# Kernel tuning notes

Measured on AMD Instinct MI355X. Metric: run time of the kernel, lower is better.

## Reference

```python
import jax, jax.numpy as jnp
import numpy as np

N_NODES = 50000
IN_CH = 512
HID = 256
HEADS = 4
N_LAYERS = 2
LN_EPS = 1e-5


def _layer_norm(x, g, b):
    mu = jnp.mean(x, axis=-1, keepdims=True)
    var = jnp.mean((x - mu) ** 2, axis=-1, keepdims=True)
    return (x - mu) * jax.lax.rsqrt(var + LN_EPS) * g + b


def _trans_conv(x, wq, bq, wk, bk, wv, bv):
    # x: [N, HID]; projections -> [N, HEADS, HID]
    N = x.shape[0]
    qs = (x @ wq + bq).reshape(N, HEADS, HID)
    ks = (x @ wk + bk).reshape(N, HEADS, HID)
    vs = (x @ wv + bv).reshape(N, HEADS, HID)
    # NOTE: global Frobenius norm, matching torch.norm(t, p=2)
    qs = qs / jnp.linalg.norm(qs)
    ks = ks / jnp.linalg.norm(ks)
    kvs = jnp.einsum('lhm,lhd->hmd', ks, vs)                 # [H, C, C]
    attn_num = jnp.einsum('nhm,hmd->nhd', qs, kvs) + N * vs  # [N, H, C]
    ks_sum = jnp.sum(ks, axis=0)                             # [H, C]
    denom = jnp.einsum('nhm,hm->nh', qs, ks_sum)[..., None] + N
    return jnp.mean(attn_num / denom, axis=1)                # [N, HID]


def setup_inputs() -> dict:
    key = jax.random.key(0)
    ks = jax.random.split(key, 32)
    s_in = 1.0 / np.sqrt(IN_CH)
    s_h = 1.0 / np.sqrt(HID)
    inp = {
        'x': jax.random.normal(ks[0], (N_NODES, IN_CH), jnp.float32),
        'fc_w': jax.random.uniform(ks[1], (IN_CH, HID), jnp.float32, -s_in, s_in),
        'fc_b': jax.random.uniform(ks[2], (HID,), jnp.float32, -s_in, s_in),
        'ln0_g': jnp.ones((HID,), jnp.float32),
        'ln0_b': jnp.zeros((HID,), jnp.float32),
    }
    for i in range(N_LAYERS):
        base = 3 + i * 8
        inp[f'wq{i}'] = jax.random.uniform(ks[base + 0], (HID, HID * HEADS), jnp.float32, -s_h, s_h)
        inp[f'bq{i}'] = jax.random.uniform(ks[base + 1], (HID * HEADS,), jnp.float32, -s_h, s_h)
        inp[f'wk{i}'] = jax.random.uniform(ks[base + 2], (HID, HID * HEADS), jnp.float32, -s_h, s_h)
        inp[f'bk{i}'] = jax.random.uniform(ks[base + 3], (HID * HEADS,), jnp.float32, -s_h, s_h)
        inp[f'wv{i}'] = jax.random.uniform(ks[base + 4], (HID, HID * HEADS), jnp.float32, -s_h, s_h)
        inp[f'bv{i}'] = jax.random.uniform(ks[base + 5], (HID * HEADS,), jnp.float32, -s_h, s_h)
        inp[f'ln{i + 1}_g'] = jnp.ones((HID,), jnp.float32)
        inp[f'ln{i + 1}_b'] = jnp.zeros((HID,), jnp.float32)
    return inp


def reference(x, fc_w, fc_b, ln0_g, ln0_b,
              wq0, bq0, wk0, bk0, wv0, bv0, ln1_g, ln1_b,
              wq1, bq1, wk1, bk1, wv1, bv1, ln2_g, ln2_b):
    # input FFN path (ffn is hard-coded True); dropout is identity in eval mode
    h = jax.nn.relu(_layer_norm(x @ fc_w + fc_b, ln0_g, ln0_b))
    layers = [(wq0, bq0, wk0, bk0, wv0, bv0, ln1_g, ln1_b),
              (wq1, bq1, wk1, bk1, wv1, bv1, ln2_g, ln2_b)]
    for (wq, bq, wk, bk, wv, bv, g, b) in layers:
        prev = h
        h = _trans_conv(h, wq, bq, wk, bk, wv, bv)
        h = (h + prev) / 2.0
        h = jax.nn.relu(_layer_norm(h, g, b))
    return h
```

## Files before the change

### kernel.cpp

```cpp
#include <hip/hip_runtime.h>

#define NN    50000
#define IN_CH 512
#define HID   256
#define PJ    1024
#define FN    50000.0f
#define KTP   50176
#define NCH   98
#define CHK   512

typedef __attribute__((ext_vector_type(4)))  float f32x4;
typedef __attribute__((ext_vector_type(16))) float f32x16;
typedef __attribute__((ext_vector_type(4)))  int   i32x4;
typedef __attribute__((ext_vector_type(8)))  unsigned short u16x8;

__device__ inline void mfma16(f32x4& c, i32x4 a, i32x4 b){
  asm("v_mfma_f32_16x16x32_bf16 %0, %1, %2, %0" : "+v"(c) : "v"(a), "v"(b));
}
__device__ inline void mfma32(f32x16& c, i32x4 a, i32x4 b){
  asm("v_mfma_f32_32x32x16_bf16 %0, %1, %2, %0" : "+v"(c) : "v"(a), "v"(b));
}

__device__ inline unsigned short f2bf(float f){
  unsigned int u = __builtin_bit_cast(unsigned int, f);
  unsigned int r = (u + 0x7fffu + ((u >> 16) & 1u)) >> 16;
  return (unsigned short)r;
}
__device__ inline float bf2f(unsigned short u){
  unsigned int x = ((unsigned int)u) << 16;
  return __builtin_bit_cast(float, x);
}

__device__ inline float wave_reduce(float v){
  #pragma unroll
  for(int o=32;o>0;o>>=1) v += __shfl_down(v,o,64);
  return v;
}
__device__ inline float block_reduce(float v, float* sh4){
  v = wave_reduce(v);
  int lane = threadIdx.x & 63, wv = threadIdx.x >> 6;
  if(lane==0) sh4[wv] = v;
  __syncthreads();
  float r = sh4[0]+sh4[1]+sh4[2]+sh4[3];
  __syncthreads();
  return r;
}

__global__ void wconv(const float* __restrict__ w, unsigned short* __restrict__ wt){
  int idx = blockIdx.x*256 + threadIdx.x;
  if(idx >= IN_CH*HID) return;
  int k = idx >> 8, n = idx & 255;
  wt[((size_t)(k>>6)*256 + n)*64 + (k&63)] = f2bf(w[idx]);
}

__global__ __launch_bounds__(512)
void ffn_gemm(const float* __restrict__ X, const unsigned short* __restrict__ FWT2,
              const float* __restrict__ bias, const float* __restrict__ g,
              const float* __restrict__ b2, unsigned short* __restrict__ hbo){
  __shared__ __align__(16) unsigned char smem[55296];
  unsigned short (*as)[72] = (unsigned short(*)[72])smem;
  unsigned short (*bs)[72] = (unsigned short(*)[72])(smem + 18432);
  int t = threadIdx.x;
  int bm = blockIdx.x*128;
  int w = t>>6, lane = t&63;
  int wr = w>>2, wc = w&3;
  f32x4 acc[4][4];
  #pragma unroll
  for(int i=0;i<4;i++)
    #pragma unroll
    for(int j=0;j<4;j++) acc[i][j] = (f32x4){0.f,0.f,0.f,0.f};

  int ar = t>>2, aq = t&3;
  bool aok = (bm+ar) < NN;
  const float* xsrc = X + (size_t)(bm+ar)*IN_CH + aq*16;
  ushort4 aregs[4];
  u16x8 bregs[4];
  #pragma unroll
  for(int i=0;i<4;i++){
    float4 v = aok ? *(const float4*)(xsrc + i*4) : make_float4(0.f,0.f,0.f,0.f);
    ushort4 u; u.x=f2bf(v.x); u.y=f2bf(v.y); u.z=f2bf(v.z); u.w=f2bf(v.w);
    aregs[i]=u;
  }
  #pragma unroll
  for(int i=0;i<4;i++) bregs[i] = *(const u16x8*)(FWT2 + (size_t)t*32 + i*8);

  for(int kb=0;kb<8;kb++){
    __syncthreads();
    #pragma unroll
    for(int i=0;i<4;i++) *(ushort4*)&as[ar][aq*16 + i*4] = aregs[i];
    { int n = t>>1, q = t&1;
      #pragma unroll
      for(int i=0;i<4;i++) *(u16x8*)&bs[n][q*32 + i*8] = bregs[i];
    }
    __syncthreads();
    if(kb<7){
      const float* xs2 = xsrc + (kb+1)*64;
      #pragma unroll
      for(int i=0;i<4;i++){
        float4 v = aok ? *(const float4*)(xs2 + i*4) : make_float4(0.f,0.f,0.f,0.f);
        ushort4 u; u.x=f2bf(v.x); u.y=f2bf(v.y); u.z=f2bf(v.z); u.w=f2bf(v.w);
        aregs[i]=u;
      }
      const unsigned short* bsrc = FWT2 + (size_t)(kb+1)*16384 + (size_t)t*32;
      #pragma unroll
      for(int i=0;i<4;i++) bregs[i] = *(const u16x8*)(bsrc + i*8);
    }
    #pragma unroll
    for(int ks=0;ks<2;ks++){
      i32x4 af[4], bfv[4];
      #pragma unroll
      for(int i=0;i<4;i++) af[i]  = *(const i32x4*)&as[wr*64 + i*16 + (lane&15)][ks*32 + (lane>>4)*8];
      #pragma unroll
      for(int j=0;j<4;j++) bfv[j] = *(const i32x4*)&bs[wc*64 + j*16 + (lane&15)][ks*32 + (lane>>4)*8];
      #pragma unroll
      for(int i=0;i<4;i++)
        #pragma unroll
        for(int j=0;j<4;j++) mfma16(acc[i][j], af[i], bfv[j]);
    }
  }
  __syncthreads();
  int cb = wc*64;
  #pragma unroll
  for(int j=0;j<4;j++){
    float bb = bias[cb + j*16 + (lane&15)];
    #pragma unroll
    for(int i=0;i<4;i++)
      #pragma unroll
      for(int r=0;r<4;r++) acc[i][j][r] += bb;
  }
  float (*lnp)[4][2] = (float(*)[4][2])smem;
  float (*lnstat)[2] = (float(*)[2])(smem + 4096);
  #pragma unroll
  for(int i=0;i<4;i++)
    #pragma unroll
    for(int r=0;r<4;r++){
      float s=0.f, q=0.f;
      #pragma unroll
      for(int j=0;j<4;j++){ float a=acc[i][j][r]; s+=a; q+=a*a; }
      #pragma unroll
      for(int m=1;m<16;m<<=1){ s += __shfl_xor(s,m,64); q += __shfl_xor(q,m,64); }
      if((lane&15)==0){
        int row = wr*64 + i*16 + (lane>>4)*4 + r;
        lnp[row][wc][0]=s; lnp[row][wc][1]=q;
      }
    }
  __syncthreads();
  if(t<128){
    float s=0.f,q=0.f;
    #pragma unroll
    for(int c=0;c<4;c++){ s+=lnp[t][c][0]; q+=lnp[t][c][1]; }
    float mu = s*(1.f/HID);
    float var = q*(1.f/HID) - mu*mu;
    lnstat[t][0]=mu; lnstat[t][1]=rsqrtf(var+1e-5f);
  }
  __syncthreads();
  #pragma unroll
  for(int j=0;j<4;j++){
    int col = cb + j*16 + (lane&15);
    float gg = g[col], bb = b2[col];
    #pragma unroll
    for(int i=0;i<4;i++)
      #pragma unroll
      for(int r=0;r<4;r++){
        int row = wr*64 + i*16 + (lane>>4)*4 + r;
        int grow = bm + row;
        if(grow<NN){
          float y = fmaxf((acc[i][j][r]-lnstat[row][0])*lnstat[row][1]*gg + bb, 0.f);
          hbo[(size_t)grow*HID + col] = f2bf(y);
        }
      }
  }
}

__global__ void ln_relu2b(const unsigned short* __restrict__ in, const float* __restrict__ g,
                          const float* __restrict__ b, unsigned short* __restrict__ outb,
                          float* __restrict__ outf, int M){
  int lane = threadIdx.x & 63, wv = threadIdx.x >> 6;
  int row = blockIdx.x*4 + wv;
  if(row>=M) return;
  const unsigned short* rp = in + (size_t)row*HID;
  ushort4 hv = *(const ushort4*)(rp + lane*4);
  float v[4] = {bf2f(hv.x), bf2f(hv.y), bf2f(hv.z), bf2f(hv.w)};
  float sum = v[0]+v[1]+v[2]+v[3];
  float sq  = v[0]*v[0]+v[1]*v[1]+v[2]*v[2]+v[3]*v[3];
  sum = wave_reduce(sum); sq = wave_reduce(sq);
  sum = __shfl(sum,0,64); sq = __shfl(sq,0,64);
  float mu = sum*(1.f/HID);
  float var = sq*(1.f/HID) - mu*mu;
  float rs = rsqrtf(var + 1e-5f);
  float y[4];
  #pragma unroll
  for(int j=0;j<4;j++){ int c=lane*4+j;
    y[j] = fmaxf((v[j]-mu)*rs*g[c] + b[c], 0.f); }
  if(outb){
    ushort4 u; u.x=f2bf(y[0]); u.y=f2bf(y[1]); u.z=f2bf(y[2]); u.w=f2bf(y[3]);
    *(ushort4*)(outb + (size_t)row*HID + lane*4) = u;
  }
  if(outf){
    float4 f; f.x=y[0]; f.y=y[1]; f.z=y[2]; f.w=y[3];
    *(float4*)(outf + (size_t)row*HID + lane*4) = f;
  }
}

__global__ __launch_bounds__(256)
void transpose_h(const unsigned short* __restrict__ hb, unsigned short* __restrict__ ht){
  __shared__ unsigned short ts[64][72];
  int r0 = blockIdx.x*64, c0 = blockIdx.y*64;
  int t = threadIdx.x;
  { int r = t&63, q = t>>6;
    #pragma unroll
    for(int i=0;i<2;i++){
      int c = q*16 + i*8;
      u16x8 v = {0,0,0,0,0,0,0,0};
      if(r0+r < NN) v = *(const u16x8*)(hb + (size_t)(r0+r)*HID + c0 + c);
      *(u16x8*)&ts[r][c] = v;
    }
  }
  __syncthreads();
  { int c = t>>2, q = t&3;
    unsigned short tmp[16];
    #pragma unroll
    for(int i=0;i<16;i++) tmp[i] = ts[q*16+i][c];
    unsigned short* dst = ht + (size_t)(c0+c)*KTP + r0 + q*16;
    *(u16x8*)(dst)   = *(u16x8*)&tmp[0];
    *(u16x8*)(dst+8) = *(u16x8*)&tmp[8];
  }
}

__global__ __launch_bounds__(256)
void gram_mfma(const unsigned short* __restrict__ ht, float* __restrict__ gp){
  const int qmap[3] = {0,1,3};
  int qi = blockIdx.x, q = qmap[qi], ch = blockIdx.y;
  __shared__ unsigned short as[128][72], bs[128][72];
  int r0 = (q>>1)*128, c0 = (q&1)*128;
  int t = threadIdx.x, w=t>>6, lane=t&63;
  int wr=w>>1, wc=w&1;
  f32x4 acc[4][4];
  #pragma unroll
  for(int i=0;i<4;i++)
    #pragma unroll
    for(int j=0;j<4;j++) acc[i][j] = (f32x4){0.f,0.f,0.f,0.f};
  size_t kbase = (size_t)ch*CHK;
  for(int k0=0;k0<CHK;k0+=64){
    { int r = t>>1, h2 = t&1;
      const unsigned short* srcA = ht + (size_t)(r0+r)*KTP + kbase + k0 + h2*32;
      const unsigned short* srcB = ht + (size_t)(c0+r)*KTP + kbase + k0 + h2*32;
      #pragma unroll
      for(int i=0;i<4;i++) *(u16x8*)&as[r][h2*32+i*8] = *(const u16x8*)(srcA + i*8);
      #pragma unroll
      for(int i=0;i<4;i++) *(u16x8*)&bs[r][h2*32+i*8] = *(const u16x8*)(srcB + i*8);
    }
    __syncthreads();
    #pragma unroll
    for(int ks=0;ks<2;ks++){
      i32x4 af[4], bfv[4];
      #pragma unroll
      for(int i=0;i<4;i++) af[i]  = *(const i32x4*)&as[wr*64 + i*16 + (lane&15)][ks*32 + (lane>>4)*8];
      #pragma unroll
      for(int j=0;j<4;j++) bfv[j] = *(const i32x4*)&bs[wc*64 + j*16 + (lane&15)][ks*32 + (lane>>4)*8];
      #pragma unroll
      for(int i=0;i<4;i++)
        #pragma unroll
        for(int j=0;j<4;j++) mfma16(acc[i][j], af[i], bfv[j]);
    }
    __syncthreads();
  }
  float* dst = gp + ((size_t)qi*NCH + ch)*16384;
  #pragma unroll
  for(int i=0;i<4;i++)
    #pragma unroll
    for(int j=0;j<4;j++)
      #pragma unroll
      for(int r=0;r<4;r++)
        dst[(wr*64+i*16+(lane>>4)*4+r)*128 + wc*64+j*16+(lane&15)] = acc[i][j][r];
}

__global__ void gram_post(const float* __restrict__ gp, float* __restrict__ G,
                          const unsigned short* __restrict__ ht, float* __restrict__ svec){
  int b = blockIdx.x;
  if(b < 192){
    int qi = b>>6; int e = (b&63)*256 + threadIdx.x;
    const float* p = gp + (size_t)qi*NCH*16384 + e;
    float s=0.f;
    for(int c=0;c<NCH;c++) s += p[(size_t)c*16384];
    int i = e>>7, j = e&127;
    int r0 = (qi==2)?128:0, c0 = (qi==0)?0:128;
    G[(r0+i)*256 + c0+j] = s;
    if(qi==1) G[(c0+j)*256 + (r0+i)] = s;
  } else {
    int row = b - 192;
    const unsigned short* p = ht + (size_t)row*KTP;
    float s = 0.f;
    for(int i = threadIdx.x*8; i < KTP; i += 2048){
      u16x8 v = *(const u16x8*)(p + i);
      #pragma unroll
      for(int e=0;e<8;e++) s += bf2f(v[e]);
    }
    __shared__ float sh4[4];
    float tot = block_reduce(s, sh4);
    if(threadIdx.x==0) svec[row] = tot;
  }
}

__global__ void gw_gemm3(const float* __restrict__ G, const float* __restrict__ Wq,
                         const float* __restrict__ Wk, const float* __restrict__ Wv,
                         float* __restrict__ gw){
  const float* B = blockIdx.z==0?Wq:(blockIdx.z==1?Wk:Wv);
  float* C = gw + (size_t)blockIdx.z*262144;
  __shared__ float As[64][33];
  __shared__ float Bs[32][64];
  int bm = blockIdx.x*64, bn = blockIdx.y*64;
  int t = threadIdx.x;
  int tn = t & 15, tm = t >> 4;
  float acc[4][4] = {};
  for(int k0=0;k0<HID;k0+=32){
    { int kk=t&31, rr=t>>5;
      #pragma unroll
      for(int p=0;p<8;p++){ int r=rr+p*8;
        As[r][kk] = G[(size_t)(bm+r)*HID + k0+kk]; } }
    { int nn=t&63, kr=t>>6;
      #pragma unroll
      for(int p=0;p<8;p++){ int k=kr+p*4;
        Bs[k][nn] = B[(size_t)(k0+k)*PJ + bn+nn]; } }
    __syncthreads();
    for(int k=0;k<32;k++){
      float a[4], b[4];
      #pragma unroll
      for(int i=0;i<4;i++) a[i]=As[tm*4+i][k];
      #pragma unroll
      for(int j=0;j<4;j++) b[j]=Bs[k][tn*4+j];
      #pragma unroll
      for(int i=0;i<4;i++)
        #pragma unroll
        for(int j=0;j<4;j++) acc[i][j] += a[i]*b[j];
    }
    __syncthreads();
  }
  #pragma unroll
  for(int i=0;i<4;i++)
    #pragma unroll
    for(int j=0;j<4;j++)
      C[(size_t)(bm+tm*4+i)*PJ + bn+tn*4+j] = acc[i][j];
}

__global__ void wtr(const float* __restrict__ Wq, const float* __restrict__ Wk,
                    const float* __restrict__ Wv, const float* __restrict__ s,
                    const float* __restrict__ gw, float* __restrict__ avec,
                    float* __restrict__ trp){
  int b = blockIdx.x;
  if(b < 12){
    int z = b>>2, by = b&3;
    const float* Wsel = (z==0)?Wq:(z==1)?Wk:Wv;
    int col = by*256 + threadIdx.x;
    __shared__ float ss[256];
    ss[threadIdx.x]=s[threadIdx.x];
    __syncthreads();
    float acc=0.f;
    for(int i=0;i<256;i++) acc += Wsel[(size_t)i*PJ + col]*ss[i];
    avec[(size_t)z*1024 + col]=acc;
  } else {
    int b2 = b-12;
    int which = b2>>6, by = b2&63;
    const float* Wsel = which ? Wk : Wq;
    const float* GW = gw + (size_t)which*262144;
    int t=threadIdx.x;
    int base = by*4096 + t;
    float sm=0.f;
    #pragma unroll
    for(int i=0;i<16;i++){ int idx=base+i*256; sm += Wsel[idx]*GW[idx]; }
    __shared__ float sh4[4];
    float r = block_reduce(sm, sh4);
    if(t==0) trp[which*64 + by] = r;
  }
}

__global__ void finalize_scalars(const float* __restrict__ trp, const float* __restrict__ bq,
                                 const float* __restrict__ bk, const float* __restrict__ avec,
                                 float* __restrict__ ksum, float* __restrict__ scal){
  __shared__ float sh4[4];
  int t=threadIdx.x;
  float pq = (t<64)? trp[t]    : 0.f;
  float pk = (t<64)? trp[64+t] : 0.f;
  float bqaq=0.f,bkak=0.f,bq2=0.f,bk2=0.f;
  #pragma unroll
  for(int p=0;p<4;p++){ int jn=t+p*256;
    float qv=bq[jn], kv=bk[jn];
    bqaq += qv*avec[jn]; bkak += kv*avec[1024+jn];
    bq2 += qv*qv; bk2 += kv*kv; }
  float tq = block_reduce(pq, sh4);
  float tk = block_reduce(pk, sh4);
  float s1 = block_reduce(bqaq, sh4);
  float s2 = block_reduce(bkak, sh4);
  float s3 = block_reduce(bq2, sh4);
  float s4 = block_reduce(bk2, sh4);
  if(t==0){
    float q2 = tq + 2.f*s1 + FN*s3;
    float k2 = tk + 2.f*s2 + FN*s4;
    scal[0] = rsqrtf(q2)*rsqrtf(k2);
  }
  #pragma unroll
  for(int p=0;p<4;p++){ int jn=t+p*256; ksum[jn] = avec[1024+jn] + FN*bk[jn]; }
}

__global__ void kvs_k(const float* __restrict__ Wk, const float* __restrict__ GWv,
                      const float* __restrict__ avec, const float* __restrict__ bk,
                      const float* __restrict__ bv, float* __restrict__ kvs){
  int hh=blockIdx.x, tile=blockIdx.y;
  int m0=(tile>>2)*64, d0=(tile&3)*64;
  __shared__ float As[32][64], Bs[32][64];
  int t=threadIdx.x, tn=t&15, tm=t>>4;
  float acc[4][4]={};
  for(int k0=0;k0<256;k0+=32){
    int kr=t>>6, cc=t&63;
    #pragma unroll
    for(int p=0;p<8;p++){
      int k=kr+p*4;
      As[k][cc] = Wk [(size_t)(k0+k)*PJ + hh*256 + m0+cc];
      Bs[k][cc] = GWv[(size_t)(k0+k)*PJ + hh*256 + d0+cc];
    }
    __syncthreads();
    for(int k=0;k<32;k++){
      float a[4], b[4];
      #pragma unroll
      for(int i=0;i<4;i++) a[i]=As[k][tm*4+i];
      #pragma unroll
      for(int j=0;j<4;j++) b[j]=Bs[k][tn*4+j];
      #pragma unroll
      for(int i=0;i<4;i++)
        #pragma unroll
        for(int j=0;j<4;j++) acc[i][j] += a[i]*b[j];
    }
    __syncthreads();
  }
  const float* ak = avec+1024; const float* av = avec+2048;
  #pragma unroll
  for(int i=0;i<4;i++)
    #pragma unroll
    for(int j=0;j<4;j++){
      int m=m0+tm*4+i, d=d0+tn*4+j;
      float akm=ak[hh*256+m], bkm=bk[hh*256+m];
      float avd=av[hh*256+d], bvd=bv[hh*256+d];
      kvs[(size_t)hh*65536 + m*256 + d] = acc[i][j] + akm*bvd + bkm*avd + FN*bkm*bvd;
    }
}

__global__ void u_gemm(const float* __restrict__ Wq, const float* __restrict__ kvs,
                       const float* __restrict__ Wv, const float* __restrict__ scal,
                       unsigned short* __restrict__ Ut2){
  int hh=blockIdx.x, tile=blockIdx.y;
  int i0=(tile>>2)*64, d0=(tile&3)*64;
  __shared__ float As[64][33]; __shared__ float Bs[32][64];
  int t=threadIdx.x, tn=t&15, tm=t>>4;
  float acc[4][4]={};
  for(int k0=0;k0<256;k0+=32){
    { int kk=t&31, rr=t>>5;
      #pragma unroll
      for(int p=0;p<8;p++){ int r=rr+p*8;
        As[r][kk] = Wq[(size_t)(i0+r)*PJ + hh*256 + k0+kk]; } }
    { int kr=t>>6, cc=t&63;
      #pragma unroll
      for(int p=0;p<8;p++){ int k=kr+p*4;
        Bs[k][cc] = kvs[(size_t)hh*65536 + (k0+k)*256 + d0+cc]; } }
    __syncthreads();
    for(int k=0;k<32;k++){
      float a[4], b[4];
      #pragma unroll
      for(int i=0;i<4;i++) a[i]=As[tm*4+i][k];
      #pragma unroll
      for(int j=0;j<4;j++) b[j]=Bs[k][tn*4+j];
      #pragma unroll
      for(int i=0;i<4;i++)
        #pragma unroll
        for(int j=0;j<4;j++) acc[i][j] += a[i]*b[j];
    }
    __syncthreads();
  }
  float sc = scal[0];
  #pragma unroll
  for(int i=0;i<4;i++)
    #pragma unroll
    for(int j=0;j<4;j++){
      int ii=i0+tm*4+i, d=d0+tn*4+j;
      float val = sc*acc[i][j] + FN*Wv[(size_t)ii*PJ + hh*256 + d];
      Ut2[((size_t)(d>>6)*4 + (ii>>6))*16384 + ((size_t)hh*64 + (d&63))*64 + (ii&63)] = f2bf(val);
    }
}

__global__ void head_vecs(const float* __restrict__ Wq, const float* __restrict__ bq,
                          const float* __restrict__ bv, const float* __restrict__ kvs,
                          const float* __restrict__ ksum, const float* __restrict__ scal,
                          float* __restrict__ uvec, float* __restrict__ wvec,
                          float* __restrict__ cvec){
  int hh=blockIdx.x, t=threadIdx.x;
  float scale=scal[0];
  __shared__ float bqs[256], kss[256];
  __shared__ float sh4[4];
  bqs[t]=bq[hh*256+t]; kss[t]=ksum[hh*256+t];
  __syncthreads();
  float su=0.f;
  for(int m=0;m<256;m++) su += bqs[m]*kvs[(size_t)hh*65536 + m*256 + t];
  uvec[hh*256+t] = scale*su + FN*bv[hh*256+t];
  float sw=0.f;
  for(int m=0;m<256;m++) sw += Wq[(size_t)t*PJ + hh*256 + m]*kss[m];
  wvec[hh*256+t] = scale*sw;
  float pc = bqs[t]*kss[t];
  float total = block_reduce(pc, sh4);
  if(t==0) cvec[hh] = scale*total + FN;
}

__global__ void denom_k(const unsigned short* __restrict__ hb, const float* __restrict__ wvec,
                        const float* __restrict__ cvec, float* __restrict__ denom, int M){
  __shared__ float wvl[1024];
  for(int i=threadIdx.x;i<1024;i+=256) wvl[i]=wvec[i];
  __syncthreads();
  int lane=threadIdx.x&63, wv=threadIdx.x>>6;
  int row=blockIdx.x*4+wv;
  if(row>=M) return;
  ushort4 hv = *(const ushort4*)(hb + (size_t)row*HID + lane*4);
  float h0=bf2f(hv.x), h1=bf2f(hv.y), h2=bf2f(hv.z), h3=bf2f(hv.w);
  float p[4];
  #pragma unroll
  for(int hh=0;hh<4;hh++){
    const float* wl = wvl + hh*256 + lane*4;
    p[hh] = h0*wl[0] + h1*wl[1] + h2*wl[2] + h3*wl[3];
  }
  #pragma unroll
  for(int hh=0;hh<4;hh++) p[hh]=wave_reduce(p[hh]);
  if(lane==0){
    #pragma unroll
    for(int hh=0;hh<4;hh++) denom[(size_t)row*4+hh] = 1.0f/(p[hh]+cvec[hh]);
  }
}

__global__ __launch_bounds__(512,4)
void attn_mfma(const unsigned short* __restrict__ hb, const unsigned short* __restrict__ Ut2,
               const float* __restrict__ uvec, const float* __restrict__ rden,
               unsigned short* __restrict__ outp){
  __shared__ __align__(16) unsigned char smem[38912];
  unsigned short (*bs)[72] = (unsigned short(*)[72])smem;
  float (*red)[64] = (float(*)[64])smem;
  float (*rsh)[4]  = (float(*)[4])(smem + 36864);
  int bm = blockIdx.x*128;
  int st = blockIdx.y;
  int t = threadIdx.x, w = t>>6, lane = t&63;
  int wr = w>>1, wc = w&1;
  int nst = t>>1, koff = (t&1)*32;

  f32x16 acc[4];
  #pragma unroll
  for(int j=0;j<4;j++)
    #pragma unroll
    for(int e=0;e<16;e++) acc[j][e]=0.f;

  { int r = t>>2, h2 = t&3;
    rsh[r][h2] = (bm+r<NN) ? rden[(size_t)(bm+r)*4+h2] : 1.0f; }

  const unsigned short* tb0 = Ut2 + (size_t)st*4*16384;
  u16x8 breg[4];
  #pragma unroll
  for(int i=0;i<4;i++) breg[i] = *(const u16x8*)(tb0 + (size_t)t*32 + i*8);

  int arow = bm + wr*32 + (lane&31); if(arow >= NN) arow = NN-1;
  const unsigned short* ap = hb + (size_t)arow*HID + (lane>>5)*8;

  #pragma unroll
  for(int kb=0;kb<4;kb++){
    __syncthreads();
    #pragma unroll
    for(int i=0;i<4;i++) *(u16x8*)&bs[nst][koff + i*8] = breg[i];
    __syncthreads();
    if(kb<3){
      const unsigned short* tn2 = Ut2 + ((size_t)st*4 + kb+1)*16384;
      #pragma unroll
      for(int i=0;i<4;i++) breg[i] = *(const u16x8*)(tn2 + (size_t)t*32 + i*8);
    }
    i32x4 a[4];
    #pragma unroll
    for(int ks=0;ks<4;ks++) a[ks] = *(const i32x4*)(ap + kb*64 + ks*16);
    #pragma unroll
    for(int ks=0;ks<4;ks++){
      int kc = ks*16 + (lane>>5)*8;
      #pragma unroll
      for(int j=0;j<4;j++){
        i32x4 b = *(const i32x4*)&bs[wc*128 + j*32 + (lane&31)][kc];
        mfma32(acc[j], a[ks], b);
      }
    }
  }
  float uv[4];
  #pragma unroll
  for(int j=0;j<4;j++)
    uv[j] = uvec[(wc*2 + (j>>1))*256 + st*64 + (j&1)*32 + (lane&31)];
  __syncthreads();
  if(wc==1){
    #pragma unroll
    for(int r=0;r<16;r++){
      int row = wr*32 + (r&3) + ((r>>2)<<3) + ((lane>>5)<<2);
      float d0 = rsh[row][2], d1 = rsh[row][3];
      red[row][lane&31]      = (acc[0][r]+uv[0])*d0 + (acc[2][r]+uv[2])*d1;
      red[row][32+(lane&31)] = (acc[1][r]+uv[1])*d0 + (acc[3][r]+uv[3])*d1;
    }
  }
  __syncthreads();
  if(wc==0){
    #pragma unroll
    for(int r=0;r<16;r++){
      int row = wr*32 + (r&3) + ((r>>2)<<3) + ((lane>>5)<<2);
      int gr = bm + row;
      if(gr < NN){
        float d0 = rsh[row][0], d1 = rsh[row][1];
        float v0 = ((acc[0][r]+uv[0])*d0 + (acc[2][r]+uv[2])*d1 + red[row][lane&31])      * 0.25f;
        float v1 = ((acc[1][r]+uv[1])*d0 + (acc[3][r]+uv[3])*d1 + red[row][32+(lane&31)]) * 0.25f;
        const unsigned short* hres = hb + (size_t)gr*HID + st*64;
        unsigned short* dst = outp + (size_t)gr*HID + st*64;
        dst[lane&31]      = f2bf((v0 + bf2f(hres[lane&31])) * 0.5f);
        dst[32+(lane&31)] = f2bf((v1 + bf2f(hres[32+(lane&31)])) * 0.5f);
      }
    }
  }
}

extern "C" void kernel_launch(void* const* d_in, const int* in_sizes, int n_in,
                              void* d_out, int out_size, void* d_ws, size_t ws_size,
                              hipStream_t stream){
  const float* x    = (const float*)d_in[0];
  const float* fc_w = (const float*)d_in[1];
  const float* fc_b = (const float*)d_in[2];
  const float* ln0g = (const float*)d_in[3];
  const float* ln0b = (const float*)d_in[4];
  float* out = (float*)d_out;

  float* W = (float*)d_ws;
  size_t o=0;
  unsigned short* hpre = (unsigned short*)(W+o); o+=(size_t)NN*HID/2;
  unsigned short* hb   = (unsigned short*)(W+o); o+=(size_t)NN*HID/2;
  unsigned short* ht   = (unsigned short*)(W+o); o+=(size_t)HID*KTP/2;
  unsigned short* FWT2 = (unsigned short*)(W+o); o+=(size_t)8*16384/2 + 8;
  unsigned short* Ut2  = (unsigned short*)(W+o); o+=(size_t)16*16384/2 + 8;
  float* gramp= W+o; o+=(size_t)3*NCH*16384;
  float* G    = W+o; o+=65536;
  float* gw   = W+o; o+=3*262144;
  float* svec = W+o; o+=256;
  float* avec = W+o; o+=3072;
  float* trp  = W+o; o+=128;
  float* scal = W+o; o+=16;
  float* ksum = W+o; o+=1024;
  float* kvs  = W+o; o+=262144;
  float* uvec = W+o; o+=1024;
  float* wvec = W+o; o+=1024;
  float* cvec = W+o; o+=8;
  float* denB = W+o; o+=(size_t)NN*4;
  (void)ws_size; (void)in_sizes; (void)n_in; (void)out_size;

  dim3 blk(256);
  wconv<<<dim3(512),blk,0,stream>>>(fc_w, FWT2);
  ffn_gemm<<<dim3(391),dim3(512),0,stream>>>(x, FWT2, fc_b, ln0g, ln0b, hb);

  for(int L=0; L<2; L++){
    const float* wq = (const float*)d_in[5+L*8+0];
    const float* bq = (const float*)d_in[5+L*8+1];
    const float* wk = (const float*)d_in[5+L*8+2];
    const float* bk = (const float*)d_in[5+L*8+3];
    const float* wv = (const float*)d_in[5+L*8+4];
    const float* bv = (const float*)d_in[5+L*8+5];
    const float* lng= (const float*)d_in[5+L*8+6];
    const float* lnb= (const float*)d_in[5+L*8+7];

    transpose_h<<<dim3(784,4),blk,0,stream>>>(hb, ht);
    gram_mfma<<<dim3(3,NCH),blk,0,stream>>>(ht, gramp);
    gram_post<<<dim3(448),blk,0,stream>>>(gramp, G, ht, svec);
    gw_gemm3<<<dim3(4,16,3),blk,0,stream>>>(G, wq, wk, wv, gw);
    wtr<<<dim3(140),blk,0,stream>>>(wq, wk, wv, svec, gw, avec, trp);
    finalize_scalars<<<dim3(1),blk,0,stream>>>(trp,bq,bk,avec,ksum,scal);
    kvs_k<<<dim3(4,16),blk,0,stream>>>(wk, gw+2*262144, avec, bk, bv, kvs);
    u_gemm<<<dim3(4,16),blk,0,stream>>>(wq, kvs, wv, scal, Ut2);
    head_vecs<<<dim3(4),blk,0,stream>>>(wq,bq,bv,kvs,ksum,scal,uvec,wvec,cvec);
    denom_k<<<dim3(12500),blk,0,stream>>>(hb, wvec, cvec, denB, NN);
    attn_mfma<<<dim3(391,4),dim3(512),0,stream>>>(hb, Ut2, uvec, denB, hpre);
    ln_relu2b<<<dim3(12500),blk,0,stream>>>(hpre, lng, lnb,
                                            L ? (unsigned short*)nullptr : hb,
                                            L ? out : (float*)nullptr, NN);
  }
}
```

Measured before the change: 483.7 us.

## Pre-swizzle U matrix into MFMA fragment order and read B from global

u_gemm now writes the projected U matrix in an order where each lane's MFMA B-fragment sits contiguously. attn_mfma therefore loads B operands straight from global/L2 instead of staging them through LDS with barriers. The grid is also transposed so the four column-strip blocks for the same row tile launch next to each other, which should improve L2 reuse of hb. This removes LDS traffic and per-k-block syncs, but issues more global loads per MFMA and relies on cache hits for the small U matrix.

```diff
diff --git a/kernel.cpp b/kernel.cpp
--- a/kernel.cpp
+++ b/kernel.cpp
@@ -446,7 +446,7 @@
 
 __global__ void u_gemm(const float* __restrict__ Wq, const float* __restrict__ kvs,
                        const float* __restrict__ Wv, const float* __restrict__ scal,
-                       unsigned short* __restrict__ Ut2){
+                       unsigned short* __restrict__ Ut3){
   int hh=blockIdx.x, tile=blockIdx.y;
   int i0=(tile>>2)*64, d0=(tile&3)*64;
   __shared__ float As[64][33]; __shared__ float Bs[32][64];
@@ -476,13 +476,20 @@
     __syncthreads();
   }
   float sc = scal[0];
+  int wcS = hh>>1;
   #pragma unroll
   for(int i=0;i<4;i++)
     #pragma unroll
     for(int j=0;j<4;j++){
       int ii=i0+tm*4+i, d=d0+tn*4+j;
       float val = sc*acc[i][j] + FN*Wv[(size_t)ii*PJ + hh*256 + d];
-      Ut2[((size_t)(d>>6)*4 + (ii>>6))*16384 + ((size_t)hh*64 + (d&63))*64 + (ii&63)] = f2bf(val);
+      int stS = d>>6, kbS = ii>>6;
+      int jS  = (hh&1)*2 + ((d>>5)&1);
+      int ksS = (ii>>4)&3;
+      int lnS = ((ii>>3)&1)*32 + (d&31);
+      int eS  = ii&7;
+      size_t idx = ((((size_t)(stS*4+kbS)*2 + wcS)*16 + jS*4 + ksS)<<9) + lnS*8 + eS;
+      Ut3[idx] = f2bf(val);
     }
 }
 
@@ -533,18 +540,15 @@
 }
 
 __global__ __launch_bounds__(512,4)
-void attn_mfma(const unsigned short* __restrict__ hb, const unsigned short* __restrict__ Ut2,
+void attn_mfma(const unsigned short* __restrict__ hb, const unsigned short* __restrict__ Ut3,
                const float* __restrict__ uvec, const float* __restrict__ rden,
                unsigned short* __restrict__ outp){
-  __shared__ __align__(16) unsigned char smem[38912];
-  unsigned short (*bs)[72] = (unsigned short(*)[72])smem;
-  float (*red)[64] = (float(*)[64])smem;
-  float (*rsh)[4]  = (float(*)[4])(smem + 36864);
-  int bm = blockIdx.x*128;
-  int st = blockIdx.y;
+  __shared__ float red[128][64];
+  __shared__ float rsh[128][4];
+  int st = blockIdx.x;
+  int bm = blockIdx.y*128;
   int t = threadIdx.x, w = t>>6, lane = t&63;
   int wr = w>>1, wc = w&1;
-  int nst = t>>1, koff = (t&1)*32;
 
   f32x16 acc[4];
   #pragma unroll
@@ -555,34 +559,20 @@
   { int r = t>>2, h2 = t&3;
     rsh[r][h2] = (bm+r<NN) ? rden[(size_t)(bm+r)*4+h2] : 1.0f; }
 
-  const unsigned short* tb0 = Ut2 + (size_t)st*4*16384;
-  u16x8 breg[4];
-  #pragma unroll
-  for(int i=0;i<4;i++) breg[i] = *(const u16x8*)(tb0 + (size_t)t*32 + i*8);
-
   int arow = bm + wr*32 + (lane&31); if(arow >= NN) arow = NN-1;
   const unsigned short* ap = hb + (size_t)arow*HID + (lane>>5)*8;
 
   #pragma unroll
   for(int kb=0;kb<4;kb++){
-    __syncthreads();
-    #pragma unroll
-    for(int i=0;i<4;i++) *(u16x8*)&bs[nst][koff + i*8] = breg[i];
-    __syncthreads();
-    if(kb<3){
-      const unsigned short* tn2 = Ut2 + ((size_t)st*4 + kb+1)*16384;
-      #pragma unroll
-      for(int i=0;i<4;i++) breg[i] = *(const u16x8*)(tn2 + (size_t)t*32 + i*8);
-    }
     i32x4 a[4];
     #pragma unroll
     for(int ks=0;ks<4;ks++) a[ks] = *(const i32x4*)(ap + kb*64 + ks*16);
+    const unsigned short* bp = Ut3 + ((((size_t)(st*4+kb)*2 + wc)*16)<<9) + (size_t)lane*8;
     #pragma unroll
     for(int ks=0;ks<4;ks++){
-      int kc = ks*16 + (lane>>5)*8;
       #pragma unroll
       for(int j=0;j<4;j++){
-        i32x4 b = *(const i32x4*)&bs[wc*128 + j*32 + (lane&31)][kc];
+        i32x4 b = *(const i32x4*)(bp + ((j*4+ks)<<9));
         mfma32(acc[j], a[ks], b);
       }
     }
@@ -636,7 +626,7 @@
   unsigned short* hb   = (unsigned short*)(W+o); o+=(size_t)NN*HID/2;
   unsigned short* ht   = (unsigned short*)(W+o); o+=(size_t)HID*KTP/2;
   unsigned short* FWT2 = (unsigned short*)(W+o); o+=(size_t)8*16384/2 + 8;
-  unsigned short* Ut2  = (unsigned short*)(W+o); o+=(size_t)16*16384/2 + 8;
+  unsigned short* Ut3  = (unsigned short*)(W+o); o+=(size_t)16*16384/2 + 8;
   float* gramp= W+o; o+=(size_t)3*NCH*16384;
   float* G    = W+o; o+=65536;
   float* gw   = W+o; o+=3*262144;
@@ -673,10 +663,10 @@
     wtr<<<dim3(140),blk,0,stream>>>(wq, wk, wv, svec, gw, avec, trp);
     finalize_scalars<<<dim3(1),blk,0,stream>>>(trp,bq,bk,avec,ksum,scal);
     kvs_k<<<dim3(4,16),blk,0,stream>>>(wk, gw+2*262144, avec, bk, bv, kvs);
-    u_gemm<<<dim3(4,16),blk,0,stream>>>(wq, kvs, wv, scal, Ut2);
+    u_gemm<<<dim3(4,16),blk,0,stream>>>(wq, kvs, wv, scal, Ut3);
     head_vecs<<<dim3(4),blk,0,stream>>>(wq,bq,bv,kvs,ksum,scal,uvec,wvec,cvec);
     denom_k<<<dim3(12500),blk,0,stream>>>(hb, wvec, cvec, denB, NN);
-    attn_mfma<<<dim3(391,4),dim3(512),0,stream>>>(hb, Ut2, uvec, denB, hpre);
+    attn_mfma<<<dim3(4,391),dim3(512),0,stream>>>(hb, Ut3, uvec, denB, hpre);
     ln_relu2b<<<dim3(12500),blk,0,stream>>>(hpre, lng, lnb,
                                             L ? (unsigned short*)nullptr : hb,
                                             L ? out : (float*)nullptr, NN);
```

Measured after the change: 501.0 us. 1.04x slower.

## Fuse denominator into attention kernel and merge scalar finalize into kvs kernel

Applied to the files above, without the earlier changes.

Removes the separate denom_k launch by having each attention block compute per-row, per-head denominators itself from hb and wvec. Also folds finalize_scalars into kvs_k as an extra block row. This drops two launches per layer plus the denominator buffer's write and read. In exchange, the denominator dot products are recomputed in each of the 4 column-stripe blocks, and each thread loops serially over 256 elements before the MFMA work starts.

```diff
diff --git a/kernel.cpp b/kernel.cpp
--- a/kernel.cpp
+++ b/kernel.cpp
@@ -374,38 +374,39 @@
   }
 }
 
-__global__ void finalize_scalars(const float* __restrict__ trp, const float* __restrict__ bq,
-                                 const float* __restrict__ bk, const float* __restrict__ avec,
-                                 float* __restrict__ ksum, float* __restrict__ scal){
-  __shared__ float sh4[4];
-  int t=threadIdx.x;
-  float pq = (t<64)? trp[t]    : 0.f;
-  float pk = (t<64)? trp[64+t] : 0.f;
-  float bqaq=0.f,bkak=0.f,bq2=0.f,bk2=0.f;
-  #pragma unroll
-  for(int p=0;p<4;p++){ int jn=t+p*256;
-    float qv=bq[jn], kv=bk[jn];
-    bqaq += qv*avec[jn]; bkak += kv*avec[1024+jn];
-    bq2 += qv*qv; bk2 += kv*kv; }
-  float tq = block_reduce(pq, sh4);
-  float tk = block_reduce(pk, sh4);
-  float s1 = block_reduce(bqaq, sh4);
-  float s2 = block_reduce(bkak, sh4);
-  float s3 = block_reduce(bq2, sh4);
-  float s4 = block_reduce(bk2, sh4);
-  if(t==0){
-    float q2 = tq + 2.f*s1 + FN*s3;
-    float k2 = tk + 2.f*s2 + FN*s4;
-    scal[0] = rsqrtf(q2)*rsqrtf(k2);
-  }
-  #pragma unroll
-  for(int p=0;p<4;p++){ int jn=t+p*256; ksum[jn] = avec[1024+jn] + FN*bk[jn]; }
-}
-
 __global__ void kvs_k(const float* __restrict__ Wk, const float* __restrict__ GWv,
                       const float* __restrict__ avec, const float* __restrict__ bk,
-                      const float* __restrict__ bv, float* __restrict__ kvs){
+                      const float* __restrict__ bv, float* __restrict__ kvs,
+                      const float* __restrict__ trp, const float* __restrict__ bq,
+                      float* __restrict__ ksum, float* __restrict__ scal){
   int hh=blockIdx.x, tile=blockIdx.y;
+  if(tile==16){
+    if(hh!=0) return;
+    __shared__ float sh4[4];
+    int t=threadIdx.x;
+    float pq = (t<64)? trp[t]    : 0.f;
+    float pk = (t<64)? trp[64+t] : 0.f;
+    float bqaq=0.f,bkak=0.f,bq2=0.f,bk2=0.f;
+    #pragma unroll
+    for(int p=0;p<4;p++){ int jn=t+p*256;
+      float qv=bq[jn], kv=bk[jn];
+      bqaq += qv*avec[jn]; bkak += kv*avec[1024+jn];
+      bq2 += qv*qv; bk2 += kv*kv; }
+    float tq = block_reduce(pq, sh4);
+    float tk = block_reduce(pk, sh4);
+    float s1 = block_reduce(bqaq, sh4);
+    float s2 = block_reduce(bkak, sh4);
+    float s3 = block_reduce(bq2, sh4);
+    float s4 = block_reduce(bk2, sh4);
+    if(t==0){
+      float q2 = tq + 2.f*s1 + FN*s3;
+      float k2 = tk + 2.f*s2 + FN*s4;
+      scal[0] = rsqrtf(q2)*rsqrtf(k2);
+    }
+    #pragma unroll
+    for(int p=0;p<4;p++){ int jn=t+p*256; ksum[jn] = avec[1024+jn] + FN*bk[jn]; }
+    return;
+  }
   int m0=(tile>>2)*64, d0=(tile&3)*64;
   __shared__ float As[32][64], Bs[32][64];
   int t=threadIdx.x, tn=t&15, tm=t>>4;
@@ -508,34 +509,10 @@
   if(t==0) cvec[hh] = scale*total + FN;
 }
 
-__global__ void denom_k(const unsigned short* __restrict__ hb, const float* __restrict__ wvec,
-                        const float* __restrict__ cvec, float* __restrict__ denom, int M){
-  __shared__ float wvl[1024];
-  for(int i=threadIdx.x;i<1024;i+=256) wvl[i]=wvec[i];
-  __syncthreads();
-  int lane=threadIdx.x&63, wv=threadIdx.x>>6;
-  int row=blockIdx.x*4+wv;
-  if(row>=M) return;
-  ushort4 hv = *(const ushort4*)(hb + (size_t)row*HID + lane*4);
-  float h0=bf2f(hv.x), h1=bf2f(hv.y), h2=bf2f(hv.z), h3=bf2f(hv.w);
-  float p[4];
-  #pragma unroll
-  for(int hh=0;hh<4;hh++){
-    const float* wl = wvl + hh*256 + lane*4;
-    p[hh] = h0*wl[0] + h1*wl[1] + h2*wl[2] + h3*wl[3];
-  }
-  #pragma unroll
-  for(int hh=0;hh<4;hh++) p[hh]=wave_reduce(p[hh]);
-  if(lane==0){
-    #pragma unroll
-    for(int hh=0;hh<4;hh++) denom[(size_t)row*4+hh] = 1.0f/(p[hh]+cvec[hh]);
-  }
-}
-
 __global__ __launch_bounds__(512,4)
 void attn_mfma(const unsigned short* __restrict__ hb, const unsigned short* __restrict__ Ut2,
-               const float* __restrict__ uvec, const float* __restrict__ rden,
-               unsigned short* __restrict__ outp){
+               const float* __restrict__ uvec, const float* __restrict__ wvec,
+               const float* __restrict__ cvec, unsigned short* __restrict__ outp){
   __shared__ __align__(16) unsigned char smem[38912];
   unsigned short (*bs)[72] = (unsigned short(*)[72])smem;
   float (*red)[64] = (float(*)[64])smem;
@@ -553,7 +530,22 @@
     for(int e=0;e<16;e++) acc[j][e]=0.f;
 
   { int r = t>>2, h2 = t&3;
-    rsh[r][h2] = (bm+r<NN) ? rden[(size_t)(bm+r)*4+h2] : 1.0f; }
+    int grow = bm + r;
+    if(grow < NN){
+      const unsigned short* hp = hb + (size_t)grow*HID;
+      const float* wp = wvec + h2*256;
+      float dot = 0.f;
+      #pragma unroll 4
+      for(int c=0;c<32;c++){
+        u16x8 hv8 = *(const u16x8*)(hp + c*8);
+        #pragma unroll
+        for(int e=0;e<8;e++) dot += bf2f(hv8[e]) * wp[c*8+e];
+      }
+      rsh[r][h2] = 1.0f/(dot + cvec[h2]);
+    } else {
+      rsh[r][h2] = 1.0f;
+    }
+  }
 
   const unsigned short* tb0 = Ut2 + (size_t)st*4*16384;
   u16x8 breg[4];
@@ -649,7 +641,6 @@
   float* uvec = W+o; o+=1024;
   float* wvec = W+o; o+=1024;
   float* cvec = W+o; o+=8;
-  float* denB = W+o; o+=(size_t)NN*4;
   (void)ws_size; (void)in_sizes; (void)n_in; (void)out_size;
 
   dim3 blk(256);
@@ -671,12 +662,11 @@
     gram_post<<<dim3(448),blk,0,stream>>>(gramp, G, ht, svec);
     gw_gemm3<<<dim3(4,16,3),blk,0,stream>>>(G, wq, wk, wv, gw);
     wtr<<<dim3(140),blk,0,stream>>>(wq, wk, wv, svec, gw, avec, trp);
-    finalize_scalars<<<dim3(1),blk,0,stream>>>(trp,bq,bk,avec,ksum,scal);
-    kvs_k<<<dim3(4,16),blk,0,stream>>>(wk, gw+2*262144, avec, bk, bv, kvs);
+    kvs_k<<<dim3(4,17),blk,0,stream>>>(wk, gw+2*262144, avec, bk, bv, kvs,
+                                       trp, bq, ksum, scal);
     u_gemm<<<dim3(4,16),blk,0,stream>>>(wq, kvs, wv, scal, Ut2);
     head_vecs<<<dim3(4),blk,0,stream>>>(wq,bq,bv,kvs,ksum,scal,uvec,wvec,cvec);
-    denom_k<<<dim3(12500),blk,0,stream>>>(hb, wvec, cvec, denB, NN);
-    attn_mfma<<<dim3(391,4),dim3(512),0,stream>>>(hb, Ut2, uvec, denB, hpre);
+    attn_mfma<<<dim3(391,4),dim3(512),0,stream>>>(hb, Ut2, uvec, wvec, cvec, hpre);
     ln_relu2b<<<dim3(12500),blk,0,stream>>>(hpre, lng, lnb,
                                             L ? (unsigned short*)nullptr : hb,
                                             L ? out : (float*)nullptr, NN);
```

New measurement: 654.2 us. 35.2% more time.
